# Optimization experiments

Measured on AMD Instinct MI355X. Metric: run time of the kernel, lower is better.

Reference implementation:

```python
import jax, jax.numpy as jnp
import numpy as np

EMBED_DIM = 1024
NUM_HEADS = 16
HEAD_DIM = EMBED_DIM // NUM_HEADS


def setup_inputs() -> dict:
    key = jax.random.key(0)
    ks = jax.random.split(key, 5)
    B, N, C = 4, 2048, EMBED_DIM
    x = jax.random.normal(ks[0], (B, N, C), dtype=jnp.float32)
    # Linear params (PyTorch layout: weight [out, in])
    s = 1.0 / np.sqrt(C)
    W_qkv = jax.random.uniform(ks[1], (3 * C, C), dtype=jnp.float32, minval=-s, maxval=s)
    b_qkv = jax.random.uniform(ks[2], (3 * C,), dtype=jnp.float32, minval=-s, maxval=s)
    W_out = jax.random.uniform(ks[3], (C, C), dtype=jnp.float32, minval=-s, maxval=s)
    b_out = jax.random.uniform(ks[4], (C,), dtype=jnp.float32, minval=-s, maxval=s)
    return {"x": x, "W_qkv": W_qkv, "b_qkv": b_qkv, "W_out": W_out, "b_out": b_out}


def _rotate_half(t):
    t1, t2 = jnp.split(t, 2, axis=-1)
    return jnp.concatenate((-t2, t1), axis=-1)


def _rope_cos_sin(seq_len, dim, dtype):
    inv_freq = 1.0 / (10000.0 ** (jnp.arange(0, dim, 2, dtype=jnp.float32) / dim))
    t = jnp.arange(seq_len, dtype=jnp.float32)
    freqs = jnp.einsum("i,j->ij", t, inv_freq)  # [N, dim/2]
    emb = jnp.concatenate((freqs, freqs), axis=-1)  # [N, dim]
    return emb.astype(dtype)


def reference(x, W_qkv, b_qkv, W_out, b_out):
    B, N, C = x.shape
    H, D = NUM_HEADS, HEAD_DIM
    qkv = x @ W_qkv.T + b_qkv  # [B, N, 3C]
    qkv = qkv.reshape(B, N, 3, H, D).transpose(2, 0, 3, 1, 4)  # [3, B, H, N, D]
    q, k, v = qkv[0], qkv[1], qkv[2]
    emb = _rope_cos_sin(N, D, x.dtype)
    cos = jnp.cos(emb)[None, None, :, :]  # [1,1,N,D]
    sin = jnp.sin(emb)[None, None, :, :]
    q = q * cos + _rotate_half(q) * sin
    k = k * cos + _rotate_half(k) * sin
    scale = D ** -0.5
    attn = jnp.einsum("bhnd,bhmd->bhnm", q, k) * scale  # [B,H,N,N]
    attn = jax.nn.softmax(attn, axis=-1)
    out = jnp.einsum("bhnm,bhmd->bhnd", attn, v)  # [B,H,N,D]
    out = out.transpose(0, 2, 1, 3).reshape(B, N, C)
    return out @ W_out.T + b_out
```

## Files before the change

### kernel.cpp

```cpp
#include <hip/hip_runtime.h>
#include <hip/hip_bf16.h>
#include <cstdint>
#include <cstddef>

#define SEQ 2048
#define NBATCH 4
#define EMB 1024
#define NH 16
#define HD 64
#define MTOT (NBATCH * SEQ)

typedef __attribute__((ext_vector_type(8))) short bf16x8;
typedef __attribute__((ext_vector_type(4))) float f32x4;
typedef __attribute__((ext_vector_type(16))) float f32x16;
typedef unsigned short u16;
typedef unsigned int u32;

__device__ __forceinline__ float bf2f(u16 v) {
  union { u32 u; float f; } c; c.u = ((u32)v) << 16; return c.f;
}
__device__ __forceinline__ u16 f2bf(float f) {
  union { float f; u32 u; } c; c.f = f;
  u32 u = c.u;
  return (u16)((u + 0x7FFFu + ((u >> 16) & 1u)) >> 16);
}
__device__ __forceinline__ u32 f2u(float f) {
  union { float f; u32 u; } c; c.f = f; return c.u;
}

__global__ void cast_kernel(const float* __restrict__ in, u16* __restrict__ out, int n4) {
  int stride = gridDim.x * blockDim.x;
  for (int i = blockIdx.x * blockDim.x + threadIdx.x; i < n4; i += stride) {
    float4 v = reinterpret_cast<const float4*>(in)[i];
    ushort4 o;
    o.x = f2bf(v.x); o.y = f2bf(v.y); o.z = f2bf(v.z); o.w = f2bf(v.w);
    reinterpret_cast<ushort4*>(out)[i] = o;
  }
}

__global__ void rope_table2_kernel(float* __restrict__ tab2) {
  int i = blockIdx.x * blockDim.x + threadIdx.x;
  if (i >= SEQ * 32) return;
  int n = i >> 5, j = i & 31;
  float invf = 1.0f / powf(10000.0f, (float)(2 * j) / 64.0f);
  float ang = (float)n * invf;
  tab2[2 * i] = cosf(ang);
  tab2[2 * i + 1] = sinf(ang);
}

__device__ __forceinline__ void gld_lds16(const u16* g, u16* l) {
  __builtin_amdgcn_global_load_lds((const __attribute__((address_space(1))) void*)g,
                                   (__attribute__((address_space(3))) void*)l, 16, 0, 0);
}

__global__ __launch_bounds__(256, 2)
void gemm_bt_f32(const u16* __restrict__ A, const u16* __restrict__ Bw,
                 const float* __restrict__ bias, float* __restrict__ Cout,
                 int N, int tiles_n) {
  __shared__ u16 lA[128 * 64];
  __shared__ u16 lB[128 * 64];
  const int K = 1024;
  int bm = blockIdx.x / tiles_n;
  int bn = blockIdx.x % tiles_n;
  int t = threadIdx.x;
  int wave = t >> 6, lane = t & 63;
  int wm = wave >> 1, wn = wave & 1;
  int l15 = lane & 15, l4 = lane >> 4;

  f32x4 acc[4][4];
#pragma unroll
  for (int i = 0; i < 4; ++i)
#pragma unroll
    for (int j = 0; j < 4; ++j) acc[i][j] = (f32x4){0.f, 0.f, 0.f, 0.f};

  int su[4], sr[4], sc[4];
#pragma unroll
  for (int i = 0; i < 4; ++i) {
    int u = (i * 4 + wave) * 64 + lane;
    su[i] = u;
    sr[i] = u >> 3;
    sc[i] = (u & 7) ^ (sr[i] & 7);
  }

  for (int kt = 0; kt < K / 64; ++kt) {
    if (kt) __syncthreads();
#pragma unroll
    for (int i = 0; i < 4; ++i) {
      gld_lds16(A + (size_t)(bm * 128 + sr[i]) * K + kt * 64 + sc[i] * 8, &lA[su[i] * 8]);
      gld_lds16(Bw + (size_t)(bn * 128 + sr[i]) * K + kt * 64 + sc[i] * 8, &lB[su[i] * 8]);
    }
    __syncthreads();
#pragma unroll
    for (int ks = 0; ks < 2; ++ks) {
      bf16x8 af[4], bfr[4];
#pragma unroll
      for (int mb = 0; mb < 4; ++mb) {
        int r = wm * 64 + mb * 16 + l15;
        int cc = (ks * 4 + l4) ^ (r & 7);
        af[mb] = *reinterpret_cast<const bf16x8*>(&lA[r * 64 + cc * 8]);
      }
#pragma unroll
      for (int nb = 0; nb < 4; ++nb) {
        int r = wn * 64 + nb * 16 + l15;
        int cc = (ks * 4 + l4) ^ (r & 7);
        bfr[nb] = *reinterpret_cast<const bf16x8*>(&lB[r * 64 + cc * 8]);
      }
#pragma unroll
      for (int mb = 0; mb < 4; ++mb)
#pragma unroll
        for (int nb = 0; nb < 4; ++nb)
          acc[mb][nb] = __builtin_amdgcn_mfma_f32_16x16x32_bf16(af[mb], bfr[nb], acc[mb][nb], 0, 0, 0);
    }
  }

#pragma unroll
  for (int mb = 0; mb < 4; ++mb)
#pragma unroll
    for (int nb = 0; nb < 4; ++nb) {
      int row0 = bm * 128 + wm * 64 + mb * 16 + l4 * 4;
      int col = bn * 128 + wn * 64 + nb * 16 + l15;
      float bv = bias[col];
#pragma unroll
      for (int r = 0; r < 4; ++r)
        Cout[(size_t)(row0 + r) * N + col] = acc[mb][nb][r] + bv;
    }
}

__global__ __launch_bounds__(256, 2)
void gemm_qkv_rope(const u16* __restrict__ A, const u16* __restrict__ Bw,
                   const float* __restrict__ bias, const float* __restrict__ tab2,
                   u16* __restrict__ Qb, u16* __restrict__ Kb, u16* __restrict__ Vtb) {
  __shared__ u16 lA[128 * 64];
  __shared__ u16 lB[128 * 64];
  const int K = 1024, tiles_n = 24;
  int bm = blockIdx.x / tiles_n;
  int bn = blockIdx.x % tiles_n;
  int t = threadIdx.x;
  int wave = t >> 6, lane = t & 63;
  int wm = wave >> 1, wn = wave & 1;
  int l15 = lane & 15, l4 = lane >> 4;

  f32x4 acc[4][4];
#pragma unroll
  for (int i = 0; i < 4; ++i)
#pragma unroll
    for (int j = 0; j < 4; ++j) acc[i][j] = (f32x4){0.f, 0.f, 0.f, 0.f};

  int su[4], sr[4], sc[4];
#pragma unroll
  for (int i = 0; i < 4; ++i) {
    int u = (i * 4 + wave) * 64 + lane;
    su[i] = u;
    sr[i] = u >> 3;
    sc[i] = (u & 7) ^ (sr[i] & 7);
  }

  for (int kt = 0; kt < K / 64; ++kt) {
    if (kt) __syncthreads();
#pragma unroll
    for (int i = 0; i < 4; ++i) {
      gld_lds16(A + (size_t)(bm * 128 + sr[i]) * K + kt * 64 + sc[i] * 8, &lA[su[i] * 8]);
      gld_lds16(Bw + (size_t)(bn * 128 + sr[i]) * K + kt * 64 + sc[i] * 8, &lB[su[i] * 8]);
    }
    __syncthreads();
#pragma unroll
    for (int ks = 0; ks < 2; ++ks) {
      bf16x8 af[4], bfr[4];
#pragma unroll
      for (int mb = 0; mb < 4; ++mb) {
        int r = wm * 64 + mb * 16 + l15;
        int cc = (ks * 4 + l4) ^ (r & 7);
        af[mb] = *reinterpret_cast<const bf16x8*>(&lA[r * 64 + cc * 8]);
      }
#pragma unroll
      for (int nb = 0; nb < 4; ++nb) {
        int r = wn * 64 + nb * 16 + l15;
        int cc = (ks * 4 + l4) ^ (r & 7);
        bfr[nb] = *reinterpret_cast<const bf16x8*>(&lB[r * 64 + cc * 8]);
      }
#pragma unroll
      for (int mb = 0; mb < 4; ++mb)
#pragma unroll
        for (int nb = 0; nb < 4; ++nb)
          acc[mb][nb] = __builtin_amdgcn_mfma_f32_16x16x32_bf16(af[mb], bfr[nb], acc[mb][nb], 0, 0, 0);
    }
  }

  int type = bn >> 3;
  int h = (bn * 2 + wn) & 15;
  int colbase = bn * 128 + wn * 64;
  float bv[4];
#pragma unroll
  for (int nb = 0; nb < 4; ++nb) bv[nb] = bias[colbase + nb * 16 + l15];

  if (type < 2) {
    u16* dst0 = (type == 0) ? Qb : Kb;
    float qs = (type == 0) ? 0.1803368801111163f : 1.0f;
#pragma unroll
    for (int mb = 0; mb < 4; ++mb) {
      int row0 = bm * 128 + wm * 64 + mb * 16 + l4 * 4;
#pragma unroll
      for (int r = 0; r < 4; ++r) {
        int row = row0 + r;
        int bb = row >> 11, nl = row & 2047;
        const float* tp = tab2 + (size_t)nl * 64;
        float2 cs  = *reinterpret_cast<const float2*>(tp + 2 * l15);
        float2 cs2 = *reinterpret_cast<const float2*>(tp + 2 * (16 + l15));
        float a0 = acc[mb][0][r] + bv[0];
        float a1 = acc[mb][1][r] + bv[1];
        float a2 = acc[mb][2][r] + bv[2];
        float a3 = acc[mb][3][r] + bv[3];
        float o0 = (a0 * cs.x  - a2 * cs.y)  * qs;
        float o2 = (a2 * cs.x  + a0 * cs.y)  * qs;
        float o1 = (a1 * cs2.x - a3 * cs2.y) * qs;
        float o3 = (a3 * cs2.x + a1 * cs2.y) * qs;
        u16* dst = dst0 + ((size_t)(bb * 16 + h) * SEQ + nl) * 64;
        dst[l15]      = f2bf(o0);
        dst[16 + l15] = f2bf(o1);
        dst[32 + l15] = f2bf(o2);
        dst[48 + l15] = f2bf(o3);
      }
    }
  } else {
#pragma unroll
    for (int mb = 0; mb < 4; ++mb) {
      int row0 = bm * 128 + wm * 64 + mb * 16 + l4 * 4;
      int bb = row0 >> 11, nl0 = row0 & 2047;
#pragma unroll
      for (int nb = 0; nb < 4; ++nb) {
        int d = nb * 16 + l15;
        ushort4 pk;
        pk.x = f2bf(acc[mb][nb][0] + bv[nb]);
        pk.y = f2bf(acc[mb][nb][1] + bv[nb]);
        pk.z = f2bf(acc[mb][nb][2] + bv[nb]);
        pk.w = f2bf(acc[mb][nb][3] + bv[nb]);
        *reinterpret_cast<ushort4*>(&Vtb[((size_t)(bb * 16 + h) * 64 + d) * SEQ + nl0]) = pk;
      }
    }
  }
}

__global__ __launch_bounds__(256, 4)
void attn_kernel(const u16* __restrict__ Q, const u16* __restrict__ Kk,
                 const u16* __restrict__ Vt, u16* __restrict__ Out) {
  int bid = blockIdx.x;
  int swz = (bid & 7) * 128 + (bid >> 3);
  int bh = swz >> 4;
  int qt = swz & 15;
  int b = bh >> 4, h = bh & 15;
  int t = threadIdx.x;
  int wave = t >> 6, lane = t & 63;
  int l31 = lane & 31, hi = lane >> 5;

  __shared__ u16 lK[2][512 * 8];
  __shared__ u16 lV[2][512 * 8];

  const u16* Qh = Q + (size_t)bh * SEQ * 64;
  const u16* Kh = Kk + (size_t)bh * SEQ * 64;
  const u16* Vh = Vt + (size_t)bh * 64 * SEQ;
  int q0w = qt * 128 + wave * 32;

  bf16x8 qf[4];
#pragma unroll
  for (int dc = 0; dc < 4; ++dc)
    qf[dc] = *reinterpret_cast<const bf16x8*>(
        &Qh[(size_t)(q0w + l31) * 64 + dc * 16 + hi * 8]);

  f32x16 oacc[2];
#pragma unroll
  for (int db = 0; db < 2; ++db)
#pragma unroll
    for (int r = 0; r < 16; ++r) oacc[db][r] = 0.f;
  float dn = 0.f;

  auto stage = [&](int buf, int kt) {
#pragma unroll
    for (int p = 0; p < 2; ++p) {
      int u = p * 256 + t;
      gld_lds16(Kh + (size_t)(kt * 64 + (u & 63)) * 64 + (u >> 6) * 8, &lK[buf][u * 8]);
      gld_lds16(Vh + (size_t)(u & 63) * SEQ + kt * 64 + (u >> 6) * 8, &lV[buf][u * 8]);
    }
  };

  union PF { u32 w[4]; bf16x8 v; };
  int cur = 0;
  stage(0, 0);
  for (int kt = 0; kt < SEQ / 64; ++kt) {
    if (kt + 1 < SEQ / 64) {
      stage(cur ^ 1, kt + 1);
      asm volatile("s_waitcnt vmcnt(4)" ::: "memory");
    } else {
      asm volatile("s_waitcnt vmcnt(0)" ::: "memory");
    }
    __builtin_amdgcn_s_barrier();

    f32x16 s[2];
#pragma unroll
    for (int cb = 0; cb < 2; ++cb)
#pragma unroll
      for (int r = 0; r < 16; ++r) s[cb][r] = 0.f;
    __builtin_amdgcn_s_setprio(1);
#pragma unroll
    for (int cb = 0; cb < 2; ++cb) {
#pragma unroll
      for (int dc = 0; dc < 4; ++dc) {
        bf16x8 kf = *reinterpret_cast<const bf16x8*>(
            &lK[cur][(((dc * 2 + hi) << 6) + cb * 32 + l31) * 8]);
        s[cb] = __builtin_amdgcn_mfma_f32_32x32x16_bf16(kf, qf[dc], s[cb], 0, 0, 0);
      }
    }
    __builtin_amdgcn_s_setprio(0);

    PF pa[2][2];
#pragma unroll
    for (int cb = 0; cb < 2; ++cb) {
#pragma unroll
      for (int r = 0; r < 16; ++r) {
        float e = __builtin_amdgcn_exp2f(s[cb][r]);
        s[cb][r] = e;
        dn += e;
      }
#pragma unroll
      for (int c = 0; c < 2; ++c) {
        u32 u0 = f2u(s[cb][8 * c + 0]) + 0x8000u;
        u32 u1 = f2u(s[cb][8 * c + 1]) + 0x8000u;
        u32 u2 = f2u(s[cb][8 * c + 2]) + 0x8000u;
        u32 u3 = f2u(s[cb][8 * c + 3]) + 0x8000u;
        u32 u4 = f2u(s[cb][8 * c + 4]) + 0x8000u;
        u32 u5 = f2u(s[cb][8 * c + 5]) + 0x8000u;
        u32 u6 = f2u(s[cb][8 * c + 6]) + 0x8000u;
        u32 u7 = f2u(s[cb][8 * c + 7]) + 0x8000u;
        u32 a1 = __builtin_amdgcn_perm(u1, u0, 0x07060302);
        u32 a2 = __builtin_amdgcn_perm(u3, u2, 0x07060302);
        u32 b1 = __builtin_amdgcn_perm(u5, u4, 0x07060302);
        u32 b2 = __builtin_amdgcn_perm(u7, u6, 0x07060302);
        asm("v_permlane32_swap_b32 %0, %1" : "+v"(a1), "+v"(b1));
        asm("v_permlane32_swap_b32 %0, %1" : "+v"(a2), "+v"(b2));
        pa[cb][c].w[0] = a1; pa[cb][c].w[1] = a2;
        pa[cb][c].w[2] = b1; pa[cb][c].w[3] = b2;
      }
    }

    __builtin_amdgcn_s_setprio(1);
#pragma unroll
    for (int cb = 0; cb < 2; ++cb)
#pragma unroll
      for (int c = 0; c < 2; ++c)
#pragma unroll
        for (int db = 0; db < 2; ++db) {
          bf16x8 vf = *reinterpret_cast<const bf16x8*>(
              &lV[cur][(((cb * 4 + c * 2 + hi) << 6) + db * 32 + l31) * 8]);
          oacc[db] = __builtin_amdgcn_mfma_f32_32x32x16_bf16(pa[cb][c].v, vf, oacc[db], 0, 0, 0);
        }
    __builtin_amdgcn_s_setprio(0);
    __builtin_amdgcn_s_barrier();
    cur ^= 1;
  }

  dn += __shfl_xor(dn, 32);
#pragma unroll
  for (int r = 0; r < 16; ++r) {
    int qrel = (r & 3) + 8 * (r >> 2) + 4 * hi;
    float dfull = __shfl(dn, qrel);
    float inv = __builtin_amdgcn_rcpf(dfull);
    int q = q0w + qrel;
#pragma unroll
    for (int db = 0; db < 2; ++db) {
      int d = db * 32 + l31;
      Out[(size_t)(b * SEQ + q) * EMB + h * 64 + d] = f2bf(oacc[db][r] * inv);
    }
  }
}

extern "C" void kernel_launch(void* const* d_in, const int* in_sizes, int n_in,
                              void* d_out, int out_size, void* d_ws, size_t ws_size,
                              hipStream_t stream) {
  const float* x = (const float*)d_in[0];
  const float* bqkv = (const float*)d_in[2];
  const float* bout = (const float*)d_in[4];
  float* out = (float*)d_out;

  char* ws = (char*)d_ws;
  size_t off = 0;
  auto alloc = [&](size_t bytes) {
    void* p = ws + off;
    off += (bytes + 255) & ~(size_t)255;
    return p;
  };
  u16* xb    = (u16*)alloc((size_t)MTOT * EMB * 2);
  u16* wqkvb = (u16*)alloc((size_t)3 * EMB * EMB * 2);
  u16* woutb = (u16*)alloc((size_t)EMB * EMB * 2);
  u16* Qb    = (u16*)alloc((size_t)64 * SEQ * HD * 2);
  u16* Kb    = (u16*)alloc((size_t)64 * SEQ * HD * 2);
  u16* Vtb   = (u16*)alloc((size_t)64 * HD * SEQ * 2);
  u16* aout  = (u16*)alloc((size_t)MTOT * EMB * 2);
  float* tab2 = (float*)alloc((size_t)SEQ * 32 * 2 * 4);
  (void)ws_size; (void)in_sizes; (void)n_in; (void)out_size;

  cast_kernel<<<2048, 256, 0, stream>>>(x, xb, MTOT * EMB / 4);
  cast_kernel<<<1024, 256, 0, stream>>>((const float*)d_in[1], wqkvb, 3 * EMB * EMB / 4);
  cast_kernel<<<512, 256, 0, stream>>>((const float*)d_in[3], woutb, EMB * EMB / 4);
  rope_table2_kernel<<<(SEQ * 32 + 255) / 256, 256, 0, stream>>>(tab2);

  gemm_qkv_rope<<<64 * 24, 256, 0, stream>>>(xb, wqkvb, bqkv, tab2, Qb, Kb, Vtb);
  attn_kernel<<<64 * 16, 256, 0, stream>>>(Qb, Kb, Vtb, aout);
  gemm_bt_f32<<<64 * 8, 256, 0, stream>>>(aout, woutb, bout, out, EMB, 8);
}
```

Baseline: 194.1 us.

## Stage K/V through registers into padded LDS instead of direct global-to-LDS loads

Swaps the direct global-to-LDS K/V staging for a register prefetch: the next tile is loaded into registers at the top of the iteration and written to the other LDS buffer after the PV MFMAs. The LDS layout gains one padding row per 64-row chunk (stride 65) so fragment reads avoid bank conflicts. One barrier per iteration now covers both the write and the reuse. The cost is more VGPRs for the prefetch registers, which may lower occupancy, plus extra LDS write instructions.

```diff
diff --git a/kernel.cpp b/kernel.cpp
--- a/kernel.cpp
+++ b/kernel.cpp
@@ -252,8 +252,8 @@
   int wave = t >> 6, lane = t & 63;
   int l31 = lane & 31, hi = lane >> 5;
 
-  __shared__ u16 lK[2][512 * 8];
-  __shared__ u16 lV[2][512 * 8];
+  __shared__ u16 lK[2][520 * 8];
+  __shared__ u16 lV[2][520 * 8];
 
   const u16* Qh = Q + (size_t)bh * SEQ * 64;
   const u16* Kh = Kk + (size_t)bh * SEQ * 64;
@@ -273,26 +273,33 @@
     for (int r = 0; r < 16; ++r) oacc[db][r] = 0.f;
   float dn = 0.f;
 
-  auto stage = [&](int buf, int kt) {
+  bf16x8 kreg[2], vreg[2];
+  auto stage_load = [&](int kt) {
 #pragma unroll
     for (int p = 0; p < 2; ++p) {
       int u = p * 256 + t;
-      gld_lds16(Kh + (size_t)(kt * 64 + (u & 63)) * 64 + (u >> 6) * 8, &lK[buf][u * 8]);
-      gld_lds16(Vh + (size_t)(u & 63) * SEQ + kt * 64 + (u >> 6) * 8, &lV[buf][u * 8]);
+      int r = u >> 3, c = u & 7;
+      kreg[p] = *reinterpret_cast<const bf16x8*>(&Kh[(size_t)(kt * 64 + r) * 64 + c * 8]);
+      vreg[p] = *reinterpret_cast<const bf16x8*>(&Vh[(size_t)r * SEQ + kt * 64 + c * 8]);
+    }
+  };
+  auto stage_write = [&](int buf) {
+#pragma unroll
+    for (int p = 0; p < 2; ++p) {
+      int u = p * 256 + t;
+      int r = u >> 3, c = u & 7;
+      *reinterpret_cast<bf16x8*>(&lK[buf][(c * 65 + r) * 8]) = kreg[p];
+      *reinterpret_cast<bf16x8*>(&lV[buf][(c * 65 + r) * 8]) = vreg[p];
     }
   };
 
   union PF { u32 w[4]; bf16x8 v; };
   int cur = 0;
-  stage(0, 0);
+  stage_load(0);
+  stage_write(0);
+  __syncthreads();
   for (int kt = 0; kt < SEQ / 64; ++kt) {
-    if (kt + 1 < SEQ / 64) {
-      stage(cur ^ 1, kt + 1);
-      asm volatile("s_waitcnt vmcnt(4)" ::: "memory");
-    } else {
-      asm volatile("s_waitcnt vmcnt(0)" ::: "memory");
-    }
-    __builtin_amdgcn_s_barrier();
+    if (kt + 1 < SEQ / 64) stage_load(kt + 1);
 
     f32x16 s[2];
 #pragma unroll
@@ -305,7 +312,7 @@
 #pragma unroll
       for (int dc = 0; dc < 4; ++dc) {
         bf16x8 kf = *reinterpret_cast<const bf16x8*>(
-            &lK[cur][(((dc * 2 + hi) << 6) + cb * 32 + l31) * 8]);
+            &lK[cur][((dc * 2 + hi) * 65 + cb * 32 + l31) * 8]);
         s[cb] = __builtin_amdgcn_mfma_f32_32x32x16_bf16(kf, qf[dc], s[cb], 0, 0, 0);
       }
     }
@@ -349,11 +356,13 @@
 #pragma unroll
         for (int db = 0; db < 2; ++db) {
           bf16x8 vf = *reinterpret_cast<const bf16x8*>(
-              &lV[cur][(((cb * 4 + c * 2 + hi) << 6) + db * 32 + l31) * 8]);
+              &lV[cur][((cb * 4 + c * 2 + hi) * 65 + db * 32 + l31) * 8]);
           oacc[db] = __builtin_amdgcn_mfma_f32_32x32x16_bf16(pa[cb][c].v, vf, oacc[db], 0, 0, 0);
         }
     __builtin_amdgcn_s_setprio(0);
-    __builtin_amdgcn_s_barrier();
+
+    if (kt + 1 < SEQ / 64) stage_write(cur ^ 1);
+    __syncthreads();
     cur ^= 1;
   }
 
```

Result: faster. 187.9 us (-3.2%).
